# Kernel optimization log

Measured on AMD Instinct MI355X. Metric: run time of the kernel, lower is better.

The kernel has to match this reference:

```python
import jax, jax.numpy as jnp
import numpy as np

N = 100000
E = 1600000
G = 512  # number of graphs for pooling


def gcn_conv(x, W, b, src, dst, n):
    # PyG GCNConv: h = x @ W; symmetric deg^{-1/2} norm; scatter-add to dst; + bias
    h = x @ W                                            # [N, out]
    deg = jax.ops.segment_sum(jnp.ones(dst.shape, h.dtype), dst, num_segments=n)
    dinv = jnp.where(deg > 0, jax.lax.rsqrt(deg), 0.0)   # [N]
    norm = dinv[src] * dinv[dst]                         # [E']
    msg = norm[:, None] * h[src]                         # gather + scale, [E', out]
    out = jax.ops.segment_sum(msg, dst, num_segments=n)  # scatter-add
    return out + b


def setup_inputs() -> dict:
    key = jax.random.key(0)
    ks = jax.random.split(key, 8)
    x = jax.random.normal(ks[0], (N, 128), dtype=jnp.float32)
    edge_index = jax.random.randint(ks[1], (2, E), 0, N, dtype=jnp.int32)
    batch_index = jnp.sort(jax.random.randint(ks[2], (N,), 0, G, dtype=jnp.int32))
    W1 = jax.random.normal(ks[3], (128, 64), dtype=jnp.float32) * 0.1
    b1 = jax.random.normal(ks[4], (64,), dtype=jnp.float32) * 0.1
    W2 = jax.random.normal(ks[5], (64, 16), dtype=jnp.float32) * 0.1
    b2 = jax.random.normal(ks[6], (16,), dtype=jnp.float32) * 0.1
    return {"x": x, "edge_index": edge_index, "batch_index": batch_index,
            "W1": W1, "b1": b1, "W2": W2, "b2": b2}


def reference(x, edge_index, batch_index, W1, b1, W2, b2):
    n = x.shape[0]
    # add self-loops (PyG GCNConv default)
    loops = jnp.arange(n, dtype=edge_index.dtype)
    src = jnp.concatenate([edge_index[0], loops])
    dst = jnp.concatenate([edge_index[1], loops])

    h = jnp.tanh(gcn_conv(x, W1, b1, src, dst, n))
    h = jnp.tanh(gcn_conv(h, W2, b2, src, dst, n))

    # global_mean_pool over batch_index
    sums = jax.ops.segment_sum(h, batch_index, num_segments=G)            # [G, C]
    cnt = jax.ops.segment_sum(jnp.ones((n,), h.dtype), batch_index, num_segments=G)
    pooled = sums / jnp.maximum(cnt, 1.0)[:, None]
    return jax.nn.sigmoid(pooled)
```

## Files before the change

kernel.cpp:

```cpp
#include <hip/hip_runtime.h>
#include <hip/hip_bf16.h>

typedef float f4 __attribute__((ext_vector_type(4)));
typedef unsigned short us;
typedef unsigned int uint32;
typedef _Float16 h16;
typedef _Float16 h16x2 __attribute__((ext_vector_type(2)));
typedef _Float16 f16x8 __attribute__((ext_vector_type(8)));
typedef float f32x4v __attribute__((ext_vector_type(4)));

union h2u { uint32 u; h16 h[2]; h16x2 v; };

#define BSH 8
#define CHUNK 4096
#define CAP 6144

__global__ __launch_bounds__(256) void bscat_k(const int* __restrict__ src, const int* __restrict__ dst,
                                               int* __restrict__ bcur, unsigned int* __restrict__ bedge,
                                               const int* __restrict__ batch, int* __restrict__ gstart,
                                               int E, int B, int N, int G, int nchunk) {
    int tid = threadIdx.x;
    if (blockIdx.x >= nchunk) {
        int i = (blockIdx.x - nchunk) * 256 + tid;
        if (i >= N) return;
        int b = batch[i];
        int prev = (i == 0) ? -1 : batch[i - 1];
        for (int g = prev + 1; g <= b; ++g) gstart[g] = i;
        if (i == N - 1) {
            for (int g = b + 1; g <= G; ++g) gstart[g] = N;
        }
        return;
    }
    __shared__ int hist[512], lbase[512], cur2[512], gb[512];
    __shared__ int sa[512], sb[512];
    __shared__ unsigned int sedge[CHUNK];
    __shared__ unsigned short posb[CHUNK];
    int base = blockIdx.x * CHUNK;
    int n = min(CHUNK, E - base);
    for (int i = tid; i < 512; i += 256) hist[i] = 0;
    __syncthreads();
    for (int i = tid; i < n; i += 256) atomicAdd(&hist[dst[base + i] >> BSH], 1);
    __syncthreads();
    #pragma unroll
    for (int k = 0; k < 2; ++k) { int i = tid + k * 256; sa[i] = hist[i]; }
    __syncthreads();
    int* c = sa; int* nx = sb;
    for (int off = 1; off < 512; off <<= 1) {
        #pragma unroll
        for (int k = 0; k < 2; ++k) { int i = tid + k * 256; nx[i] = c[i] + (i >= off ? c[i - off] : 0); }
        __syncthreads();
        int* t = c; c = nx; nx = t;
    }
    #pragma unroll
    for (int k = 0; k < 2; ++k) {
        int i = tid + k * 256;
        int ex = c[i] - hist[i];
        lbase[i] = ex; cur2[i] = ex;
        if (i < B) gb[i] = hist[i] ? (i * CAP + atomicAdd(&bcur[i], hist[i])) : 0;
    }
    for (int t = tid; t < B; t += 256) {
        int e0 = lbase[t], e1 = e0 + hist[t];
        for (int j = e0; j < e1; ++j) posb[j] = (unsigned short)t;
    }
    __syncthreads();
    for (int i = tid; i < n; i += 256) {
        int d = dst[base + i];
        int s = src[base + i];
        int b = d >> BSH;
        int p = atomicAdd(&cur2[b], 1);
        sedge[p] = ((unsigned int)s << BSH) | (unsigned int)(d & ((1 << BSH) - 1));
    }
    __syncthreads();
    for (int i = tid; i < n; i += 256) {
        int b = posb[i];
        bedge[gb[b] + (i - lbase[b])] = sedge[i];
    }
}

__global__ __launch_bounds__(256) void bcsr_k(const unsigned int* __restrict__ bedge,
                                              const int* __restrict__ bcur,
                                              int* __restrict__ row_ptr, int* __restrict__ cnt,
                                              float* __restrict__ dinv, int* __restrict__ col,
                                              int N, int B) {
    __shared__ int hist[256], lofs[256], cur2[256];
    __shared__ int sa[256], sb[256];
    __shared__ int cols[CAP];
    int b = blockIdx.x, tid = threadIdx.x;
    int node0 = b << BSH;
    int g0 = b * CAP;
    int n = min(bcur[b], CAP);
    hist[tid] = 0;
    __syncthreads();
    for (int i = tid; i < n; i += 256) atomicAdd(&hist[bedge[g0 + i] & 255], 1);
    __syncthreads();
    sa[tid] = hist[tid];
    __syncthreads();
    int* c = sa; int* nx = sb;
    for (int off = 1; off < 256; off <<= 1) {
        nx[tid] = c[tid] + (tid >= off ? c[tid - off] : 0);
        __syncthreads();
        int* t = c; c = nx; nx = t;
    }
    int ex = c[tid] - hist[tid];
    lofs[tid] = ex; cur2[tid] = ex;
    int node = node0 + tid;
    if (node < N) {
        int deg = hist[tid];
        cnt[node] = deg;
        row_ptr[node] = g0 + ex;
        dinv[node] = rsqrtf((float)(deg + 1));
    }
    __syncthreads();
    for (int i = tid; i < n; i += 256) {
        unsigned int e = bedge[g0 + i];
        int p = atomicAdd(&cur2[e & 255], 1);
        if (p < CAP) cols[p] = (int)(e >> BSH);
    }
    __syncthreads();
    for (int i = tid; i < n; i += 256) col[g0 + i] = (i < CAP) ? cols[i] : 0;
}

__global__ __launch_bounds__(256) void gemm1_k(const float* __restrict__ x, const float* __restrict__ W1,
                                               const float* __restrict__ dinv, h16* __restrict__ hsh, int N) {
    __shared__ h16 xS[64][136];
    __shared__ h16 wS[8192];
    const int tid = threadIdx.x;
    const int row0 = blockIdx.x * 64;

    #pragma unroll
    for (int i = 0; i < 32; ++i) {
        int idx = tid + i * 256;
        int k = idx >> 6, cc = idx & 63;
        wS[(((k >> 3) * 64) + cc) * 8 + (k & 7)] = (h16)W1[idx];
    }
    #pragma unroll
    for (int it = 0; it < 8; ++it) {
        int i = tid + it * 256;
        int r = i >> 5;
        int k4 = (i & 31) * 4;
        int row = row0 + r;
        f4 v = (f4)(0.0f);
        if (row < N) v = *(const f4*)(x + (size_t)row * 128 + k4);
        xS[r][k4 + 0] = (h16)v.x; xS[r][k4 + 1] = (h16)v.y;
        xS[r][k4 + 2] = (h16)v.z; xS[r][k4 + 3] = (h16)v.w;
    }
    __syncthreads();

    const int wv = tid >> 6;
    const int lane = tid & 63;
    const int q = lane >> 4;
    const int c = lane & 15;
    f32x4v acc0 = {0.f, 0.f, 0.f, 0.f}, acc1 = acc0, acc2 = acc0, acc3 = acc0;
    #pragma unroll
    for (int kb = 0; kb < 4; ++kb) {
        f16x8 a = *(const f16x8*)&xS[wv * 16 + c][kb * 32 + q * 8];
        const h16* wb = &wS[(size_t)((kb * 4 + q) * 64) * 8];
        f16x8 b0 = *(const f16x8*)&wb[(0 * 16 + c) * 8];
        f16x8 b1 = *(const f16x8*)&wb[(1 * 16 + c) * 8];
        f16x8 b2 = *(const f16x8*)&wb[(2 * 16 + c) * 8];
        f16x8 b3 = *(const f16x8*)&wb[(3 * 16 + c) * 8];
        acc0 = __builtin_amdgcn_mfma_f32_16x16x32_f16(a, b0, acc0, 0, 0, 0);
        acc1 = __builtin_amdgcn_mfma_f32_16x16x32_f16(a, b1, acc1, 0, 0, 0);
        acc2 = __builtin_amdgcn_mfma_f32_16x16x32_f16(a, b2, acc2, 0, 0, 0);
        acc3 = __builtin_amdgcn_mfma_f32_16x16x32_f16(a, b3, acc3, 0, 0, 0);
    }
    #pragma unroll
    for (int j = 0; j < 4; ++j) {
        int row = row0 + wv * 16 + q * 4 + j;
        if (row < N) {
            float di = dinv[row];
            size_t base = (size_t)row * 64;
            hsh[base +  0 + c] = (h16)(acc0[j] * di);
            hsh[base + 16 + c] = (h16)(acc1[j] * di);
            hsh[base + 32 + c] = (h16)(acc2[j] * di);
            hsh[base + 48 + c] = (h16)(acc3[j] * di);
        }
    }
}

__global__ __launch_bounds__(256) void agg1_k(const h16* __restrict__ hsh, const int* __restrict__ row_ptr,
                                              const int* __restrict__ cnt, const int* __restrict__ col,
                                              const float* __restrict__ dinv, const float* __restrict__ b1,
                                              const float* __restrict__ W2, h16* __restrict__ h2sh, int N) {
    int wid = blockIdx.x * 4 + (threadIdx.x >> 6);
    int lane = threadIdx.x & 63;
    if (wid >= N) return;
    const int c16 = lane & 15;
    const int hh  = lane >> 4;
    float wreg[16];
    #pragma unroll
    for (int k = 0; k < 16; ++k) wreg[k] = W2[(hh * 16 + k) * 16 + c16];
    float bias = b1[lane];

    const int c2 = lane & 31;
    const int h  = lane >> 5;
    const uint32* rowbase = (const uint32*)hsh + c2;

    int beg = row_ptr[wid];
    int num = cnt[wid];
    float accx = 0.0f, accy = 0.0f;
    for (int e0 = 0; e0 < num; e0 += 64) {
        int rem = num - e0;
        int el = 0;
        if (lane < rem) el = col[beg + e0 + lane];
        int m = rem < 64 ? rem : 64;
        int e = 0;
        for (; e + 16 <= m; e += 16) {
            int s0 = __shfl(el, e + h);
            int s1 = __shfl(el, e + 2 + h);
            int s2 = __shfl(el, e + 4 + h);
            int s3 = __shfl(el, e + 6 + h);
            int s4 = __shfl(el, e + 8 + h);
            int s5 = __shfl(el, e + 10 + h);
            int s6 = __shfl(el, e + 12 + h);
            int s7 = __shfl(el, e + 14 + h);
            h2u u0, u1, u2, u3, u4, u5, u6, u7;
            u0.u = rowbase[(size_t)s0 * 32];
            u1.u = rowbase[(size_t)s1 * 32];
            u2.u = rowbase[(size_t)s2 * 32];
            u3.u = rowbase[(size_t)s3 * 32];
            u4.u = rowbase[(size_t)s4 * 32];
            u5.u = rowbase[(size_t)s5 * 32];
            u6.u = rowbase[(size_t)s6 * 32];
            u7.u = rowbase[(size_t)s7 * 32];
            h16x2 t01 = u0.v + u1.v;
            h16x2 t23 = u2.v + u3.v;
            h16x2 t45 = u4.v + u5.v;
            h16x2 t67 = u6.v + u7.v;
            h16x2 t03 = t01 + t23;
            h16x2 t47 = t45 + t67;
            h16x2 tt  = t03 + t47;
            accx += (float)tt[0];
            accy += (float)tt[1];
        }
        for (; e + 8 <= m; e += 8) {
            int s0 = __shfl(el, e + h);
            int s1 = __shfl(el, e + 2 + h);
            int s2 = __shfl(el, e + 4 + h);
            int s3 = __shfl(el, e + 6 + h);
            h2u u0, u1, u2, u3;
            u0.u = rowbase[(size_t)s0 * 32];
            u1.u = rowbase[(size_t)s1 * 32];
            u2.u = rowbase[(size_t)s2 * 32];
            u3.u = rowbase[(size_t)s3 * 32];
            accx += ((float)u0.h[0] + (float)u1.h[0]) + ((float)u2.h[0] + (float)u3.h[0]);
            accy += ((float)u0.h[1] + (float)u1.h[1]) + ((float)u2.h[1] + (float)u3.h[1]);
        }
        for (; e + 4 <= m; e += 4) {
            int s0 = __shfl(el, e + h);
            int s1 = __shfl(el, e + 2 + h);
            h2u u0, u1;
            u0.u = rowbase[(size_t)s0 * 32];
            u1.u = rowbase[(size_t)s1 * 32];
            accx += (float)u0.h[0] + (float)u1.h[0];
            accy += (float)u0.h[1] + (float)u1.h[1];
        }
        for (; e + 2 <= m; e += 2) {
            int s = __shfl(el, e + h);
            h2u u; u.u = rowbase[(size_t)s * 32];
            accx += (float)u.h[0];
            accy += (float)u.h[1];
        }
        if (e < m) {
            int s = __shfl(el, e);
            if (h == 0) {
                h2u u; u.u = rowbase[(size_t)s * 32];
                accx += (float)u.h[0];
                accy += (float)u.h[1];
            }
        }
    }
    accx += __shfl_xor(accx, 32);
    accy += __shfl_xor(accy, 32);
    float ra = __shfl(accx, lane >> 1);
    float rb = __shfl(accy, lane >> 1);
    float acc = (lane & 1) ? rb : ra;

    float di = dinv[wid];
    float self = (float)hsh[(size_t)wid * 64 + lane];
    float h1v = tanhf(di * (acc + self) + bias);

    float p = 0.0f;
    #pragma unroll
    for (int k = 0; k < 16; ++k) {
        float hv = __shfl(h1v, hh * 16 + k);
        p += hv * wreg[k];
    }
    p += __shfl_xor(p, 16);
    p += __shfl_xor(p, 32);
    if (lane < 16) h2sh[(size_t)wid * 16 + lane] = (h16)(di * p);
}

__global__ __launch_bounds__(256) void agg2_k(const h16* __restrict__ h2sh, const int* __restrict__ row_ptr,
                                              const int* __restrict__ cnt, const int* __restrict__ col,
                                              const float* __restrict__ dinv, const float* __restrict__ b2,
                                              h16* __restrict__ h2h, int N) {
    int t = blockIdx.x * 256 + threadIdx.x;
    int node = t >> 4;
    int c = t & 15;
    int sub = (threadIdx.x >> 4) & 3;
    if (node >= N) return;
    int beg = row_ptr[node];
    int num = cnt[node];
    float acc = 0.0f;
    for (int e0 = 0; e0 < num; e0 += 16) {
        int rem = num - e0;
        int el = 0;
        if (c < rem) el = col[beg + e0 + c];
        int m = rem < 16 ? rem : 16;
        int e = 0;
        for (; e + 4 <= m; e += 4) {
            int s0 = __shfl(el, (sub << 4) + e + 0);
            int s1 = __shfl(el, (sub << 4) + e + 1);
            int s2 = __shfl(el, (sub << 4) + e + 2);
            int s3 = __shfl(el, (sub << 4) + e + 3);
            float v0 = (float)h2sh[(size_t)s0 * 16 + c];
            float v1 = (float)h2sh[(size_t)s1 * 16 + c];
            float v2 = (float)h2sh[(size_t)s2 * 16 + c];
            float v3 = (float)h2sh[(size_t)s3 * 16 + c];
            acc += (v0 + v1) + (v2 + v3);
        }
        for (; e < m; ++e) {
            int s = __shfl(el, (sub << 4) + e);
            acc += (float)h2sh[(size_t)s * 16 + c];
        }
    }
    float di = dinv[node];
    float self = (float)h2sh[(size_t)node * 16 + c];
    h2h[(size_t)node * 16 + c] = (h16)tanhf(di * (acc + self) + b2[c]);
}

__global__ __launch_bounds__(256) void pool_seg_k(const h16* __restrict__ h2h, const int* __restrict__ gstart,
                                                  float* __restrict__ out) {
    __shared__ float sd[16][16];
    int g = blockIdx.x;
    int beg = gstart[g], end = gstart[g + 1];
    int tid = threadIdx.x;
    int c = tid & 15, r = tid >> 4;
    float acc = 0.0f;
    for (int i = beg + r; i < end; i += 16)
        acc += (float)h2h[(size_t)i * 16 + c];
    sd[r][c] = acc;
    __syncthreads();
    if (r < 8) sd[r][c] += sd[r + 8][c];
    __syncthreads();
    if (r < 4) sd[r][c] += sd[r + 4][c];
    __syncthreads();
    if (r < 2) sd[r][c] += sd[r + 2][c];
    __syncthreads();
    if (r == 0) {
        float m = (sd[0][c] + sd[1][c]) / fmaxf((float)(end - beg), 1.0f);
        out[g * 16 + c] = 1.0f / (1.0f + expf(-m));
    }
}

extern "C" void kernel_launch(void* const* d_in, const int* in_sizes, int n_in,
                              void* d_out, int out_size, void* d_ws, size_t ws_size,
                              hipStream_t stream) {
    const float* x     = (const float*)d_in[0];
    const int*   ei    = (const int*)d_in[1];
    const int*   batch = (const int*)d_in[2];
    const float* W1    = (const float*)d_in[3];
    const float* b1    = (const float*)d_in[4];
    const float* W2    = (const float*)d_in[5];
    const float* b2    = (const float*)d_in[6];
    float* out = (float*)d_out;

    const int N = in_sizes[2];
    const int E = in_sizes[1] / 2;
    const int G = out_size / 16;
    const int* src = ei;
    const int* dst = ei + E;

    const int B = (N + 255) >> 8;
    const int nchunk = (E + CHUNK - 1) / CHUNK;
    const int nbound = (N + 255) / 256;

    char* w = (char*)d_ws;
    int*   bcur     = (int*)w;    w += 512 * 4;
    int*   row_ptr  = (int*)w;    w += (size_t)N * 4;
    int*   cnt      = (int*)w;    w += (size_t)N * 4;
    float* dinv     = (float*)w;  w += (size_t)N * 4;
    int*   gstart   = (int*)w;    w += 528 * 4;
    int*   col      = (int*)w;    w += (size_t)B * CAP * 4;
    h16*   hsh      = (h16*)w;    w += (size_t)N * 64 * 2;
    h16*   h2sh     = (h16*)w;    w += (size_t)N * 16 * 2;
    h16*   h2h      = (h16*)w;    w += (size_t)N * 16 * 2;
    unsigned int* bedge = (unsigned int*)w;  w += (size_t)B * CAP * 4;

    hipMemsetAsync(bcur, 0, 512 * 4, stream);

    bscat_k <<<nchunk + nbound, 256, 0, stream>>>(src, dst, bcur, bedge, batch, gstart, E, B, N, G, nchunk);
    bcsr_k  <<<B, 256, 0, stream>>>(bedge, bcur, row_ptr, cnt, dinv, col, N, B);

    gemm1_k <<<(N + 63) / 64, 256, 0, stream>>>(x, W1, dinv, hsh, N);
    agg1_k  <<<(N + 3) / 4, 256, 0, stream>>>(hsh, row_ptr, cnt, col, dinv, b1, W2, h2sh, N);
    agg2_k  <<<((size_t)N * 16 + 255) / 256, 256, 0, stream>>>(h2sh, row_ptr, cnt, col, dinv, b2, h2h, N);
    pool_seg_k<<<G, 256, 0, stream>>>(h2h, gstart, out);
}
```

Measured before the change: 139.8 us.

## Fuse bucket CSR build with first-layer GEMM into one kernel

Merges the per-bucket CSR construction kernel and the x@W1 MFMA GEMM into a single kernel. Each block builds its 256-node CSR bucket, keeps the computed dinv in shared memory, then reuses a union of the shared buffers to run four 64-row GEMM tiles for the same nodes. This removes one launch and the global dinv reload. In exchange the GEMM runs on only B≈391 blocks instead of about 1563, so parallelism drops. The union shared footprint is also larger, which may lower occupancy.

```diff
diff --git a/kernel.cpp b/kernel.cpp
--- a/kernel.cpp
+++ b/kernel.cpp
@@ -2,7 +2,6 @@
 #include <hip/hip_bf16.h>
 
 typedef float f4 __attribute__((ext_vector_type(4)));
-typedef unsigned short us;
 typedef unsigned int uint32;
 typedef _Float16 h16;
 typedef _Float16 h16x2 __attribute__((ext_vector_type(2)));
@@ -77,104 +76,111 @@
     }
 }
 
-__global__ __launch_bounds__(256) void bcsr_k(const unsigned int* __restrict__ bedge,
-                                              const int* __restrict__ bcur,
-                                              int* __restrict__ row_ptr, int* __restrict__ cnt,
-                                              float* __restrict__ dinv, int* __restrict__ col,
-                                              int N, int B) {
-    __shared__ int hist[256], lofs[256], cur2[256];
-    __shared__ int sa[256], sb[256];
-    __shared__ int cols[CAP];
+union SharedU {
+    struct { int hist[256], cur2[256], sa[256], sb[256]; int cols[CAP]; } p1;
+    struct { h16 xS[64][136]; h16 wS[8192]; } p2;
+};
+
+__global__ __launch_bounds__(256) void bcsrgemm_k(const unsigned int* __restrict__ bedge,
+                                                  const int* __restrict__ bcur,
+                                                  const float* __restrict__ x, const float* __restrict__ W1,
+                                                  int* __restrict__ row_ptr, int* __restrict__ cnt,
+                                                  float* __restrict__ dinv, int* __restrict__ col,
+                                                  h16* __restrict__ hsh, int N, int B) {
+    __shared__ SharedU su;
+    __shared__ float sdinv[256];
     int b = blockIdx.x, tid = threadIdx.x;
     int node0 = b << BSH;
     int g0 = b * CAP;
     int n = min(bcur[b], CAP);
-    hist[tid] = 0;
-    __syncthreads();
-    for (int i = tid; i < n; i += 256) atomicAdd(&hist[bedge[g0 + i] & 255], 1);
-    __syncthreads();
-    sa[tid] = hist[tid];
-    __syncthreads();
-    int* c = sa; int* nx = sb;
+
+    su.p1.hist[tid] = 0;
+    __syncthreads();
+    for (int i = tid; i < n; i += 256) atomicAdd(&su.p1.hist[bedge[g0 + i] & 255], 1);
+    __syncthreads();
+    su.p1.sa[tid] = su.p1.hist[tid];
+    __syncthreads();
+    int* c = su.p1.sa; int* nx = su.p1.sb;
     for (int off = 1; off < 256; off <<= 1) {
         nx[tid] = c[tid] + (tid >= off ? c[tid - off] : 0);
         __syncthreads();
         int* t = c; c = nx; nx = t;
     }
-    int ex = c[tid] - hist[tid];
-    lofs[tid] = ex; cur2[tid] = ex;
+    int ex = c[tid] - su.p1.hist[tid];
+    su.p1.cur2[tid] = ex;
     int node = node0 + tid;
-    if (node < N) {
-        int deg = hist[tid];
-        cnt[node] = deg;
-        row_ptr[node] = g0 + ex;
-        dinv[node] = rsqrtf((float)(deg + 1));
+    {
+        int deg = su.p1.hist[tid];
+        float di = rsqrtf((float)(deg + 1));
+        sdinv[tid] = di;
+        if (node < N) {
+            cnt[node] = deg;
+            row_ptr[node] = g0 + ex;
+            dinv[node] = di;
+        }
     }
     __syncthreads();
     for (int i = tid; i < n; i += 256) {
         unsigned int e = bedge[g0 + i];
-        int p = atomicAdd(&cur2[e & 255], 1);
-        if (p < CAP) cols[p] = (int)(e >> BSH);
-    }
-    __syncthreads();
-    for (int i = tid; i < n; i += 256) col[g0 + i] = (i < CAP) ? cols[i] : 0;
-}
-
-__global__ __launch_bounds__(256) void gemm1_k(const float* __restrict__ x, const float* __restrict__ W1,
-                                               const float* __restrict__ dinv, h16* __restrict__ hsh, int N) {
-    __shared__ h16 xS[64][136];
-    __shared__ h16 wS[8192];
-    const int tid = threadIdx.x;
-    const int row0 = blockIdx.x * 64;
+        int p = atomicAdd(&su.p1.cur2[e & 255], 1);
+        if (p < CAP) su.p1.cols[p] = (int)(e >> BSH);
+    }
+    __syncthreads();
+    for (int i = tid; i < n; i += 256) col[g0 + i] = (i < CAP) ? su.p1.cols[i] : 0;
+    __syncthreads();
 
     #pragma unroll
     for (int i = 0; i < 32; ++i) {
         int idx = tid + i * 256;
         int k = idx >> 6, cc = idx & 63;
-        wS[(((k >> 3) * 64) + cc) * 8 + (k & 7)] = (h16)W1[idx];
-    }
-    #pragma unroll
-    for (int it = 0; it < 8; ++it) {
-        int i = tid + it * 256;
-        int r = i >> 5;
-        int k4 = (i & 31) * 4;
-        int row = row0 + r;
-        f4 v = (f4)(0.0f);
-        if (row < N) v = *(const f4*)(x + (size_t)row * 128 + k4);
-        xS[r][k4 + 0] = (h16)v.x; xS[r][k4 + 1] = (h16)v.y;
-        xS[r][k4 + 2] = (h16)v.z; xS[r][k4 + 3] = (h16)v.w;
-    }
-    __syncthreads();
-
+        su.p2.wS[(((k >> 3) * 64) + cc) * 8 + (k & 7)] = (h16)W1[idx];
+    }
     const int wv = tid >> 6;
     const int lane = tid & 63;
     const int q = lane >> 4;
-    const int c = lane & 15;
-    f32x4v acc0 = {0.f, 0.f, 0.f, 0.f}, acc1 = acc0, acc2 = acc0, acc3 = acc0;
-    #pragma unroll
-    for (int kb = 0; kb < 4; ++kb) {
-        f16x8 a = *(const f16x8*)&xS[wv * 16 + c][kb * 32 + q * 8];
-        const h16* wb = &wS[(size_t)((kb * 4 + q) * 64) * 8];
-        f16x8 b0 = *(const f16x8*)&wb[(0 * 16 + c) * 8];
-        f16x8 b1 = *(const f16x8*)&wb[(1 * 16 + c) * 8];
-        f16x8 b2 = *(const f16x8*)&wb[(2 * 16 + c) * 8];
-        f16x8 b3 = *(const f16x8*)&wb[(3 * 16 + c) * 8];
-        acc0 = __builtin_amdgcn_mfma_f32_16x16x32_f16(a, b0, acc0, 0, 0, 0);
-        acc1 = __builtin_amdgcn_mfma_f32_16x16x32_f16(a, b1, acc1, 0, 0, 0);
-        acc2 = __builtin_amdgcn_mfma_f32_16x16x32_f16(a, b2, acc2, 0, 0, 0);
-        acc3 = __builtin_amdgcn_mfma_f32_16x16x32_f16(a, b3, acc3, 0, 0, 0);
-    }
-    #pragma unroll
-    for (int j = 0; j < 4; ++j) {
-        int row = row0 + wv * 16 + q * 4 + j;
-        if (row < N) {
-            float di = dinv[row];
-            size_t base = (size_t)row * 64;
-            hsh[base +  0 + c] = (h16)(acc0[j] * di);
-            hsh[base + 16 + c] = (h16)(acc1[j] * di);
-            hsh[base + 32 + c] = (h16)(acc2[j] * di);
-            hsh[base + 48 + c] = (h16)(acc3[j] * di);
-        }
+    const int cc16 = lane & 15;
+    for (int t = 0; t < 4; ++t) {
+        int trow0 = node0 + t * 64;
+        #pragma unroll
+        for (int it = 0; it < 8; ++it) {
+            int i = tid + it * 256;
+            int r = i >> 5;
+            int k4 = (i & 31) * 4;
+            int row = trow0 + r;
+            f4 v = (f4)(0.0f);
+            if (row < N) v = *(const f4*)(x + (size_t)row * 128 + k4);
+            su.p2.xS[r][k4 + 0] = (h16)v.x; su.p2.xS[r][k4 + 1] = (h16)v.y;
+            su.p2.xS[r][k4 + 2] = (h16)v.z; su.p2.xS[r][k4 + 3] = (h16)v.w;
+        }
+        __syncthreads();
+        f32x4v acc0 = {0.f, 0.f, 0.f, 0.f}, acc1 = acc0, acc2 = acc0, acc3 = acc0;
+        #pragma unroll
+        for (int kb = 0; kb < 4; ++kb) {
+            f16x8 a = *(const f16x8*)&su.p2.xS[wv * 16 + cc16][kb * 32 + q * 8];
+            const h16* wb = &su.p2.wS[(size_t)((kb * 4 + q) * 64) * 8];
+            f16x8 b0 = *(const f16x8*)&wb[(0 * 16 + cc16) * 8];
+            f16x8 b1 = *(const f16x8*)&wb[(1 * 16 + cc16) * 8];
+            f16x8 b2 = *(const f16x8*)&wb[(2 * 16 + cc16) * 8];
+            f16x8 b3 = *(const f16x8*)&wb[(3 * 16 + cc16) * 8];
+            acc0 = __builtin_amdgcn_mfma_f32_16x16x32_f16(a, b0, acc0, 0, 0, 0);
+            acc1 = __builtin_amdgcn_mfma_f32_16x16x32_f16(a, b1, acc1, 0, 0, 0);
+            acc2 = __builtin_amdgcn_mfma_f32_16x16x32_f16(a, b2, acc2, 0, 0, 0);
+            acc3 = __builtin_amdgcn_mfma_f32_16x16x32_f16(a, b3, acc3, 0, 0, 0);
+        }
+        #pragma unroll
+        for (int j = 0; j < 4; ++j) {
+            int lrow = t * 64 + wv * 16 + q * 4 + j;
+            int row = node0 + lrow;
+            if (row < N) {
+                float di = sdinv[lrow];
+                size_t bo = (size_t)row * 64;
+                hsh[bo +  0 + cc16] = (h16)(acc0[j] * di);
+                hsh[bo + 16 + cc16] = (h16)(acc1[j] * di);
+                hsh[bo + 32 + cc16] = (h16)(acc2[j] * di);
+                hsh[bo + 48 + cc16] = (h16)(acc3[j] * di);
+            }
+        }
+        __syncthreads();
     }
 }
 
@@ -390,10 +396,9 @@
 
     hipMemsetAsync(bcur, 0, 512 * 4, stream);
 
-    bscat_k <<<nchunk + nbound, 256, 0, stream>>>(src, dst, bcur, bedge, batch, gstart, E, B, N, G, nchunk);
-    bcsr_k  <<<B, 256, 0, stream>>>(bedge, bcur, row_ptr, cnt, dinv, col, N, B);
-
-    gemm1_k <<<(N + 63) / 64, 256, 0, stream>>>(x, W1, dinv, hsh, N);
+    bscat_k   <<<nchunk + nbound, 256, 0, stream>>>(src, dst, bcur, bedge, batch, gstart, E, B, N, G, nchunk);
+    bcsrgemm_k<<<B, 256, 0, stream>>>(bedge, bcur, x, W1, row_ptr, cnt, dinv, col, hsh, N, B);
+
     agg1_k  <<<(N + 3) / 4, 256, 0, stream>>>(hsh, row_ptr, cnt, col, dinv, b1, W2, h2sh, N);
     agg2_k  <<<((size_t)N * 16 + 255) / 256, 256, 0, stream>>>(h2sh, row_ptr, cnt, col, dinv, b2, h2h, N);
     pool_seg_k<<<G, 256, 0, stream>>>(h2h, gstart, out);
```

Measured after the change: 140.6 us (median of 2 runs). About the same (+0.5%).
